# Optimization experiments

Hardware: AMD Instinct MI355X
Metric: run time of the kernel (lower is better)

Reference implementation:

```python
import math
import jax, jax.numpy as jnp
import numpy as np

H = 16  # head_count
D = 1024  # model_dim
DH = D // H  # dim_per_head = 64
PAD_IDX = 1


def setup_inputs() -> dict:
    key = jax.random.key(0)
    ks = jax.random.split(key, 16)
    B, L = 4, 512
    s = 0.02
    inp = {
        'key': jax.random.normal(ks[0], (B, L, D), jnp.float32),
        'value': jax.random.normal(ks[1], (B, L, D), jnp.float32),
        'query': jax.random.normal(ks[2], (B, L, D), jnp.float32),
        'ast_parents_matrix': jax.random.randint(ks[3], (B, L, L), 0, 200, jnp.int32),
        'mask': jnp.zeros((B, 1, L), jnp.bool_),
        'Wq': jax.random.normal(ks[4], (D, D), jnp.float32) * s,
        'bq': jnp.zeros((D,), jnp.float32),
        'Wk': jax.random.normal(ks[5], (D, D), jnp.float32) * s,
        'bk': jnp.zeros((D,), jnp.float32),
        'Wv': jax.random.normal(ks[6], (D, D), jnp.float32) * s,
        'bv': jnp.zeros((D,), jnp.float32),
        'Wo': jax.random.normal(ks[7], (D, D), jnp.float32) * s,
        'bo': jnp.zeros((D,), jnp.float32),
        'struct_emb': jax.random.normal(ks[8], (200, DH), jnp.float32).at[PAD_IDX].set(0.0),
        'value_emb': jax.random.normal(ks[9], (10000, DH), jnp.float32).at[PAD_IDX].set(0.0),
    }
    return inp


def _parent_embeddings(matrix, struct_emb, value_emb):
    # matrix: (B, Lq, K) int ids; even key positions use structure vocab, odd use value vocab
    B, Lq, K = matrix.shape
    s_ids = matrix[:, :, ::2]   # (B, Lq, ceil(K/2))
    v_ids = matrix[:, :, 1::2]  # (B, Lq, floor(K/2))
    emb_s = struct_emb[s_ids]   # (B, Lq, S, DH)
    emb_v = value_emb[v_ids]    # (B, Lq, V, DH)
    S = emb_s.shape[2]
    if emb_v.shape[2] != S:  # odd K: pad value stream by one zero slot, drop after interleave
        emb_v = jnp.concatenate([emb_v, jnp.zeros_like(emb_s[:, :, :1])], axis=2)
    pe = jnp.stack([emb_s, emb_v], axis=3).reshape(B, Lq, 2 * S, DH)
    return pe[:, :, :K, :]  # (B, Lq, K, DH)


def reference(key, value, query, ast_parents_matrix, mask,
              Wq, bq, Wk, bk, Wv, bv, Wo, bo, struct_emb, value_emb):
    B, L, _ = query.shape

    def shape(x):
        return x.reshape(B, -1, H, DH).transpose(0, 2, 1, 3)  # (B,H,L,DH)

    q = shape(query @ Wq + bq) / math.sqrt(DH)
    k = shape(key @ Wk + bk)
    v = shape(value @ Wv + bv)

    qk = jnp.einsum('bhid,bhjd->bhij', q, k)  # (B,H,L,L)

    pe = _parent_embeddings(ast_parents_matrix[:, :, :L], struct_emb, value_emb)
    score_ast = jnp.einsum('bhid,bijd->bhij', q, pe)

    scores = (qk + score_ast).astype(jnp.float32)
    scores = jnp.where(mask[:, None, :, :], -1e18, scores)  # mask: (B,1,L)->(B,1,1,L)
    attn = jax.nn.softmax(scores, axis=-1).astype(q.dtype)
    # dropout p=0.0 (eval) -> identity
    context = jnp.einsum('bhij,bhjd->bhid', attn, v)  # (B,H,L,DH)
    context = context.transpose(0, 2, 1, 3).reshape(B, L, D)
    output = context @ Wo + bo
    return output, attn
```

## Files before the change

### kernel.cpp

```cpp
#include <hip/hip_runtime.h>
#include <cstddef>

#define H 16
#define D 1024
#define DH 64
#define L 512

typedef __attribute__((ext_vector_type(8))) short bf16x8;
typedef __attribute__((ext_vector_type(4))) short bf16x4;
typedef __attribute__((ext_vector_type(4))) float f32x4;

__device__ inline short f2bf(float x) {
    union { float f; unsigned u; } c; c.f = x;
    unsigned r = (c.u + 0x7FFFu + ((c.u >> 16) & 1u)) >> 16;
    return (short)r;
}
__device__ inline float bf2f(short x) {
    union { float f; unsigned u; } c;
    c.u = ((unsigned)(unsigned short)x) << 16; return c.f;
}

__device__ inline void gload_lds16(const void* g, void* l) {
    __builtin_amdgcn_global_load_lds(
        (const __attribute__((address_space(1))) unsigned int*)g,
        (__attribute__((address_space(3))) unsigned int*)l,
        16, 0, 0);
}

struct CvtArgs { const float* src[5]; short* dst[5]; int n[5]; };

__global__ __launch_bounds__(256) void cvt_kernel(CvtArgs a) {
    int r = blockIdx.y;
    const float* s = a.src[r];
    short* d = a.dst[r];
    int n = a.n[r];
    int i = (blockIdx.x * 256 + threadIdx.x) * 8;
    if (i >= n) return;
    float4 x0 = *(const float4*)(s + i);
    float4 x1 = *(const float4*)(s + i + 4);
    bf16x8 o;
    o[0] = f2bf(x0.x); o[1] = f2bf(x0.y); o[2] = f2bf(x0.z); o[3] = f2bf(x0.w);
    o[4] = f2bf(x1.x); o[5] = f2bf(x1.y); o[6] = f2bf(x1.z); o[7] = f2bf(x1.w);
    *(bf16x8*)(d + i) = o;
}

struct WtArgs { const float* W[4]; short* T[4]; };

__global__ __launch_bounds__(256) void wtrans_kernel(WtArgs a) {
    const float* W = a.W[blockIdx.z];
    short* T = a.T[blockIdx.z];
    int idx = blockIdx.x * 256 + threadIdx.x;
    int n = idx & 1023;
    int k0 = (idx >> 10) << 3;
    bf16x8 o;
    #pragma unroll
    for (int kk = 0; kk < 8; ++kk)
        o[kk] = f2bf(W[(size_t)(k0 + kk) * 1024 + n]);
    *(bf16x8*)(T + (size_t)n * 1024 + k0) = o;
}

#define BM 128
#define BN 64
#define BKK 64

struct GemmBatch {
    const short* A[3]; const short* Bt[3]; const float* bias[3];
    void* out[3]; float scale[3]; int mode[3];
};

__global__ __launch_bounds__(256) void gemm_mfma_kernel(GemmBatch P, int M, int N, int K) {
    const int z = blockIdx.z;
    const short* __restrict__ A  = P.A[z];
    const short* __restrict__ Bt = P.Bt[z];
    const float* __restrict__ bias = P.bias[z];
    const float scale = P.scale[z];
    const int mode = P.mode[z];

    __shared__ short lds[(BM + BN) * BKK];
    short* As = lds;
    short* Bs = lds + BM * BKK;

    const int tid = threadIdx.x;
    const int wave = tid >> 6, lane = tid & 63;
    const int fm = lane & 15, quad = lane >> 4;
    const int m0 = blockIdx.y * BM, n0 = blockIdx.x * BN;

    int arow[4], acol[4];
    #pragma unroll
    for (int t = 0; t < 4; ++t) {
        int s = (wave * 4 + t) * 64 + lane;
        int row = s >> 3;
        int u = (s & 7) ^ (row & 7);
        arow[t] = row; acol[t] = u * 8;
    }
    int brow[2], bcol[2];
    #pragma unroll
    for (int t = 0; t < 2; ++t) {
        int s = (wave * 2 + t) * 64 + lane;
        int row = s >> 3;
        int u = (s & 7) ^ (row & 7);
        brow[t] = row; bcol[t] = u * 8;
    }

    int aoff[2][2], boff[4][2];
    #pragma unroll
    for (int mt = 0; mt < 2; ++mt)
        #pragma unroll
        for (int kst = 0; kst < 2; ++kst) {
            int row = wave * 32 + mt * 16 + fm;
            int u = quad + 4 * kst;
            aoff[mt][kst] = row * 64 + ((u ^ (row & 7)) * 8);
        }
    #pragma unroll
    for (int nt = 0; nt < 4; ++nt)
        #pragma unroll
        for (int kst = 0; kst < 2; ++kst) {
            int row = nt * 16 + fm;
            int u = quad + 4 * kst;
            boff[nt][kst] = row * 64 + ((u ^ (row & 7)) * 8);
        }

    f32x4 acc[2][4];
    #pragma unroll
    for (int mt = 0; mt < 2; ++mt)
        #pragma unroll
        for (int nt = 0; nt < 4; ++nt) acc[mt][nt] = (f32x4){0.f, 0.f, 0.f, 0.f};

    for (int k0 = 0; k0 < K; k0 += BKK) {
        __syncthreads();
        #pragma unroll
        for (int t = 0; t < 4; ++t)
            gload_lds16(A + (size_t)(m0 + arow[t]) * K + k0 + acol[t],
                        As + (wave * 4 + t) * 512);
        #pragma unroll
        for (int t = 0; t < 2; ++t)
            gload_lds16(Bt + (size_t)(n0 + brow[t]) * K + k0 + bcol[t],
                        Bs + (wave * 2 + t) * 512);
        __syncthreads();
        #pragma unroll
        for (int kst = 0; kst < 2; ++kst) {
            bf16x8 af[2], bfr[4];
            af[0] = *(const bf16x8*)(As + aoff[0][kst]);
            af[1] = *(const bf16x8*)(As + aoff[1][kst]);
            #pragma unroll
            for (int nt = 0; nt < 4; ++nt)
                bfr[nt] = *(const bf16x8*)(Bs + boff[nt][kst]);
            #pragma unroll
            for (int mt = 0; mt < 2; ++mt)
                #pragma unroll
                for (int nt = 0; nt < 4; ++nt)
                    acc[mt][nt] = __builtin_amdgcn_mfma_f32_16x16x32_bf16(
                        af[mt], bfr[nt], acc[mt][nt], 0, 0, 0);
        }
    }

    if (mode == 2) {
        __syncthreads();
        short (*T)[BM + 8] = (short(*)[BM + 8])&lds[0];
        #pragma unroll
        for (int mt = 0; mt < 2; ++mt)
            #pragma unroll
            for (int nt = 0; nt < 4; ++nt) {
                int nn = nt * 16 + fm;
                float bv = bias[n0 + nn];
                #pragma unroll
                for (int r = 0; r < 4; ++r) {
                    int mm = wave * 32 + mt * 16 + quad * 4 + r;
                    T[nn][mm] = f2bf((acc[mt][nt][r] + bv) * scale);
                }
            }
        __syncthreads();
        int b = m0 >> 9;
        int ibase = m0 & (L - 1);
        int hblk = n0 >> 6;
        int n = tid >> 2, seg = (tid & 3) * 32;
        short* dst = (short*)P.out[z] + (((size_t)(b * H + hblk) * DH + n) * L) + ibase + seg;
        #pragma unroll
        for (int c = 0; c < 4; ++c)
            *(bf16x8*)(dst + c * 8) = *(const bf16x8*)(&T[n][seg + c * 8]);
    } else {
        #pragma unroll
        for (int mt = 0; mt < 2; ++mt)
            #pragma unroll
            for (int nt = 0; nt < 4; ++nt) {
                int n = n0 + nt * 16 + fm;
                float bv = bias[n];
                #pragma unroll
                for (int r = 0; r < 4; ++r) {
                    int m = m0 + wave * 32 + mt * 16 + quad * 4 + r;
                    float val = (acc[mt][nt][r] + bv) * scale;
                    if (mode == 0) {
                        ((float*)P.out[z])[(size_t)m * N + n] = val;
                    } else {
                        int b = m >> 9, i = m & (L - 1);
                        int h = n >> 6, d = n & (DH - 1);
                        ((short*)P.out[z])[(((size_t)(b * H + h) * L + i) * DH) + d] = f2bf(val);
                    }
                }
            }
    }
}

__global__ __launch_bounds__(256) void ast_kernel(
    const short* __restrict__ Qb, const int* __restrict__ mat,
    const short* __restrict__ semb, const short* __restrict__ vemb,
    short* __restrict__ Sast)
{
    const int i = blockIdx.x, b = blockIdx.y;
    const int tid = threadIdx.x;
    const int wave = tid >> 6, lane = tid & 63;
    const int fm = lane & 15, quad = lane >> 4;
    __shared__ short Sl[H][L + 8];

    const short* qp = Qb + (((size_t)(b * H + fm) * L + i) * DH);
    bf16x8 a0 = *(const bf16x8*)(qp + quad * 8);
    bf16x8 a1 = *(const bf16x8*)(qp + 32 + quad * 8);

    const int* mrow = mat + ((size_t)b * L + i) * L;

    for (int jt = wave; jt < L / 16; jt += 4) {
        int j = jt * 16 + fm;
        int idx = mrow[j];
        const short* er = ((j & 1) ? vemb : semb) + (size_t)idx * DH;
        bf16x8 b0 = *(const bf16x8*)(er + quad * 8);
        bf16x8 b1 = *(const bf16x8*)(er + 32 + quad * 8);
        f32x4 c = {0.f, 0.f, 0.f, 0.f};
        c = __builtin_amdgcn_mfma_f32_16x16x32_bf16(a0, b0, c, 0, 0, 0);
        c = __builtin_amdgcn_mfma_f32_16x16x32_bf16(a1, b1, c, 0, 0, 0);
        #pragma unroll
        for (int r = 0; r < 4; ++r)
            Sl[quad * 4 + r][j] = f2bf(c[r]);
    }
    __syncthreads();
    int hh = tid >> 4, j0 = (tid & 15) * 32;
    short* dst = Sast + ((((size_t)b * L + i) * H + hh) * L) + j0;
    #pragma unroll
    for (int c = 0; c < 4; ++c)
        *(bf16x8*)(dst + c * 8) = *(const bf16x8*)(&Sl[hh][j0 + c * 8]);
}

__global__ __launch_bounds__(256) void attn_fused_kernel(
    const short* __restrict__ Qb, const short* __restrict__ Kb,
    const short* __restrict__ Vt, const short* __restrict__ Sast,
    const unsigned char* __restrict__ mask,
    float* __restrict__ attn, short* __restrict__ ctx)
{
    const int i0 = blockIdx.x * 16;
    const int h = blockIdx.y;
    const int b = blockIdx.z;
    const int tid = threadIdx.x;
    const int wave = tid >> 6, lane = tid & 63;
    const int fm = lane & 15, quad = lane >> 4;

    __shared__ short Pb[16][L + 8];
    __shared__ float red_m[4][16];
    __shared__ float red_l[4][16];

    const short* qp = Qb + (((size_t)(b * H + h) * L + i0 + fm) * DH);
    bf16x8 a0 = *(const bf16x8*)(qp + quad * 8);
    bf16x8 a1 = *(const bf16x8*)(qp + 32 + quad * 8);
    const short* Kbase = Kb + ((size_t)(b * H + h) * L) * DH;
    const short* Sb = Sast + (((size_t)b * L + i0) * H + h) * L;

    float s[8][4];
    float mx[4] = {-3.0e38f, -3.0e38f, -3.0e38f, -3.0e38f};

    #pragma unroll
    for (int t = 0; t < 8; ++t) {
        int jt = wave + t * 4;
        int j = jt * 16 + fm;
        const short* kr = Kbase + (size_t)j * DH;
        bf16x8 b0 = *(const bf16x8*)(kr + quad * 8);
        bf16x8 b1 = *(const bf16x8*)(kr + 32 + quad * 8);
        f32x4 c = {0.f, 0.f, 0.f, 0.f};
        c = __builtin_amdgcn_mfma_f32_16x16x32_bf16(a0, b0, c, 0, 0, 0);
        c = __builtin_amdgcn_mfma_f32_16x16x32_bf16(a1, b1, c, 0, 0, 0);
        bool mk = mask[(size_t)b * L + j] != 0;
        #pragma unroll
        for (int r = 0; r < 4; ++r) {
            int ir = quad * 4 + r;
            float sv = c[r] + bf2f(Sb[(size_t)ir * H * L + j]);
            sv = mk ? -1e18f : sv;
            s[t][r] = sv;
            mx[r] = fmaxf(mx[r], sv);
        }
    }

    #pragma unroll
    for (int off = 1; off <= 8; off <<= 1)
        #pragma unroll
        for (int r = 0; r < 4; ++r)
            mx[r] = fmaxf(mx[r], __shfl_xor(mx[r], off));
    if (fm == 0)
        #pragma unroll
        for (int r = 0; r < 4; ++r) red_m[wave][quad * 4 + r] = mx[r];
    __syncthreads();
    float M_[4];
    #pragma unroll
    for (int r = 0; r < 4; ++r) {
        int ir = quad * 4 + r;
        M_[r] = fmaxf(fmaxf(red_m[0][ir], red_m[1][ir]),
                      fmaxf(red_m[2][ir], red_m[3][ir]));
    }

    float sum[4] = {0.f, 0.f, 0.f, 0.f};
    #pragma unroll
    for (int t = 0; t < 8; ++t)
        #pragma unroll
        for (int r = 0; r < 4; ++r) {
            float e = __expf(s[t][r] - M_[r]);
            s[t][r] = e;
            sum[r] += e;
        }
    #pragma unroll
    for (int off = 1; off <= 8; off <<= 1)
        #pragma unroll
        for (int r = 0; r < 4; ++r)
            sum[r] += __shfl_xor(sum[r], off);
    if (fm == 0)
        #pragma unroll
        for (int r = 0; r < 4; ++r) red_l[wave][quad * 4 + r] = sum[r];
    __syncthreads();
    float inv[4];
    #pragma unroll
    for (int r = 0; r < 4; ++r) {
        int ir = quad * 4 + r;
        inv[r] = 1.f / (red_l[0][ir] + red_l[1][ir] + red_l[2][ir] + red_l[3][ir]);
    }

    #pragma unroll
    for (int t = 0; t < 8; ++t) {
        int j = (wave + t * 4) * 16 + fm;
        #pragma unroll
        for (int r = 0; r < 4; ++r) {
            int ir = quad * 4 + r;
            float p = s[t][r] * inv[r];
            attn[(((size_t)(b * H + h) * L + i0 + ir) * L) + j] = p;
            Pb[ir][j] = f2bf(p);
        }
    }
    __syncthreads();

    const short* Vb = Vt + (((size_t)(b * H + h) * DH + wave * 16 + fm) * L);
    f32x4 o = {0.f, 0.f, 0.f, 0.f};
    for (int ks = 0; ks < L; ks += 32) {
        bf16x8 pa = *(const bf16x8*)(&Pb[fm][ks + quad * 8]);
        bf16x8 vb = *(const bf16x8*)(Vb + ks + quad * 8);
        o = __builtin_amdgcn_mfma_f32_16x16x32_bf16(pa, vb, o, 0, 0, 0);
    }
    #pragma unroll
    for (int r = 0; r < 4; ++r)
        ctx[((size_t)b * L + i0 + quad * 4 + r) * D + h * DH + wave * 16 + fm] = f2bf(o[r]);
}

extern "C" void kernel_launch(void* const* d_in, const int* in_sizes, int n_in,
                              void* d_out, int out_size, void* d_ws, size_t ws_size,
                              hipStream_t stream) {
    const float* key_in   = (const float*)d_in[0];
    const float* value_in = (const float*)d_in[1];
    const float* query_in = (const float*)d_in[2];
    const int*   mat      = (const int*)d_in[3];
    const unsigned char* mask = (const unsigned char*)d_in[4];
    const float* Wq = (const float*)d_in[5];
    const float* bq = (const float*)d_in[6];
    const float* Wk = (const float*)d_in[7];
    const float* bk = (const float*)d_in[8];
    const float* Wv = (const float*)d_in[9];
    const float* bv = (const float*)d_in[10];
    const float* Wo = (const float*)d_in[11];
    const float* bo = (const float*)d_in[12];
    const float* struct_emb = (const float*)d_in[13];
    const float* value_emb  = (const float*)d_in[14];

    const int B = in_sizes[2] / (L * D);
    const int M = B * L;

    short* p = (short*)d_ws;
    short* xk  = p;  p += (size_t)M * D;
    short* xv  = p;  p += (size_t)M * D;
    short* xq  = p;  p += (size_t)M * D;
    short* WqT = p;  p += (size_t)D * D;
    short* WkT = p;  p += (size_t)D * D;
    short* WvT = p;  p += (size_t)D * D;
    short* WoT = p;  p += (size_t)D * D;
    short* semb = p; p += 16384;
    short* vemb = p; p += (size_t)in_sizes[14];
    short* Qb = p;   p += (size_t)M * D;
    short* Kb = p;   p += (size_t)M * D;
    short* Vt = p;   p += (size_t)M * D;
    short* Sast = p; p += (size_t)B * L * H * L;
    short* ctx = xk;

    float* out_p  = (float*)d_out;
    float* attn_p = out_p + (size_t)M * D;

    CvtArgs ca;
    ca.src[0] = key_in;     ca.dst[0] = xk;   ca.n[0] = M * D;
    ca.src[1] = value_in;   ca.dst[1] = xv;   ca.n[1] = M * D;
    ca.src[2] = query_in;   ca.dst[2] = xq;   ca.n[2] = M * D;
    ca.src[3] = struct_emb; ca.dst[3] = semb; ca.n[3] = in_sizes[13];
    ca.src[4] = value_emb;  ca.dst[4] = vemb; ca.n[4] = in_sizes[14];
    cvt_kernel<<<dim3((M * D) / 2048, 5), 256, 0, stream>>>(ca);

    WtArgs wa;
    wa.W[0] = Wq; wa.W[1] = Wk; wa.W[2] = Wv; wa.W[3] = Wo;
    wa.T[0] = WqT; wa.T[1] = WkT; wa.T[2] = WvT; wa.T[3] = WoT;
    wtrans_kernel<<<dim3(512, 1, 4), 256, 0, stream>>>(wa);

    GemmBatch qkv;
    qkv.A[0] = xq; qkv.Bt[0] = WqT; qkv.bias[0] = bq; qkv.out[0] = Qb; qkv.scale[0] = 0.125f; qkv.mode[0] = 1;
    qkv.A[1] = xk; qkv.Bt[1] = WkT; qkv.bias[1] = bk; qkv.out[1] = Kb; qkv.scale[1] = 1.0f;   qkv.mode[1] = 1;
    qkv.A[2] = xv; qkv.Bt[2] = WvT; qkv.bias[2] = bv; qkv.out[2] = Vt; qkv.scale[2] = 1.0f;   qkv.mode[2] = 2;
    gemm_mfma_kernel<<<dim3(D / BN, M / BM, 3), 256, 0, stream>>>(qkv, M, D, D);

    ast_kernel<<<dim3(L, B), 256, 0, stream>>>(Qb, mat, semb, vemb, Sast);

    attn_fused_kernel<<<dim3(L / 16, H, B), 256, 0, stream>>>(
        Qb, Kb, Vt, Sast, mask, attn_p, ctx);

    GemmBatch fin;
    fin.A[0] = ctx; fin.Bt[0] = WoT; fin.bias[0] = bo; fin.out[0] = out_p; fin.scale[0] = 1.0f; fin.mode[0] = 0;
    fin.A[1] = ctx; fin.Bt[1] = WoT; fin.bias[1] = bo; fin.out[1] = out_p; fin.scale[1] = 1.0f; fin.mode[1] = 0;
    fin.A[2] = ctx; fin.Bt[2] = WoT; fin.bias[2] = bo; fin.out[2] = out_p; fin.scale[2] = 1.0f; fin.mode[2] = 0;
    gemm_mfma_kernel<<<dim3(D / BN, M / BM, 1), 256, 0, stream>>>(fin, M, D, D);
}
```

Measured before the change: 242.0 us.

## Double attention row tile, stage AST scores in LDS, merge prep kernels, batch gathers

```diff
diff --git a/kernel.cpp b/kernel.cpp
--- a/kernel.cpp
+++ b/kernel.cpp
@@ -27,36 +27,38 @@
         16, 0, 0);
 }
 
-struct CvtArgs { const float* src[5]; short* dst[5]; int n[5]; };
-
-__global__ __launch_bounds__(256) void cvt_kernel(CvtArgs a) {
-    int r = blockIdx.y;
-    const float* s = a.src[r];
-    short* d = a.dst[r];
-    int n = a.n[r];
-    int i = (blockIdx.x * 256 + threadIdx.x) * 8;
-    if (i >= n) return;
-    float4 x0 = *(const float4*)(s + i);
-    float4 x1 = *(const float4*)(s + i + 4);
-    bf16x8 o;
-    o[0] = f2bf(x0.x); o[1] = f2bf(x0.y); o[2] = f2bf(x0.z); o[3] = f2bf(x0.w);
-    o[4] = f2bf(x1.x); o[5] = f2bf(x1.y); o[6] = f2bf(x1.z); o[7] = f2bf(x1.w);
-    *(bf16x8*)(d + i) = o;
-}
-
-struct WtArgs { const float* W[4]; short* T[4]; };
-
-__global__ __launch_bounds__(256) void wtrans_kernel(WtArgs a) {
-    const float* W = a.W[blockIdx.z];
-    short* T = a.T[blockIdx.z];
-    int idx = blockIdx.x * 256 + threadIdx.x;
-    int n = idx & 1023;
-    int k0 = (idx >> 10) << 3;
-    bf16x8 o;
-    #pragma unroll
-    for (int kk = 0; kk < 8; ++kk)
-        o[kk] = f2bf(W[(size_t)(k0 + kk) * 1024 + n]);
-    *(bf16x8*)(T + (size_t)n * 1024 + k0) = o;
+struct PrepArgs {
+    const float* csrc[5]; short* cdst[5]; int cn[5];
+    const float* W[4]; short* T[4];
+};
+
+__global__ __launch_bounds__(256) void prep_kernel(PrepArgs a) {
+    const int y = blockIdx.y;
+    if (y < 5) {
+        const float* s = a.csrc[y];
+        short* d = a.cdst[y];
+        int n = a.cn[y];
+        int i = (blockIdx.x * 256 + threadIdx.x) * 8;
+        if (i >= n) return;
+        float4 x0 = *(const float4*)(s + i);
+        float4 x1 = *(const float4*)(s + i + 4);
+        bf16x8 o;
+        o[0] = f2bf(x0.x); o[1] = f2bf(x0.y); o[2] = f2bf(x0.z); o[3] = f2bf(x0.w);
+        o[4] = f2bf(x1.x); o[5] = f2bf(x1.y); o[6] = f2bf(x1.z); o[7] = f2bf(x1.w);
+        *(bf16x8*)(d + i) = o;
+    } else {
+        const float* W = a.W[y - 5];
+        short* T = a.T[y - 5];
+        int idx = blockIdx.x * 256 + threadIdx.x;
+        if (idx >= 1024 * 128) return;
+        int n = idx & 1023;
+        int k0 = (idx >> 10) << 3;
+        bf16x8 o;
+        #pragma unroll
+        for (int kk = 0; kk < 8; ++kk)
+            o[kk] = f2bf(W[(size_t)(k0 + kk) * 1024 + n]);
+        *(bf16x8*)(T + (size_t)n * 1024 + k0) = o;
+    }
 }
 
 #define BM 128
@@ -218,12 +220,24 @@
 
     const int* mrow = mat + ((size_t)b * L + i) * L;
 
-    for (int jt = wave; jt < L / 16; jt += 4) {
-        int j = jt * 16 + fm;
-        int idx = mrow[j];
-        const short* er = ((j & 1) ? vemb : semb) + (size_t)idx * DH;
-        bf16x8 b0 = *(const bf16x8*)(er + quad * 8);
-        bf16x8 b1 = *(const bf16x8*)(er + 32 + quad * 8);
+    int idxs[8];
+    const short* ebase[8];
+    #pragma unroll
+    for (int t = 0; t < 8; ++t) {
+        int j = (wave + t * 4) * 16 + fm;
+        idxs[t] = mrow[j];
+    }
+    #pragma unroll
+    for (int t = 0; t < 8; ++t) {
+        int j = (wave + t * 4) * 16 + fm;
+        ebase[t] = ((j & 1) ? vemb : semb) + (size_t)idxs[t] * DH;
+    }
+
+    #pragma unroll
+    for (int t = 0; t < 8; ++t) {
+        int j = (wave + t * 4) * 16 + fm;
+        bf16x8 b0 = *(const bf16x8*)(ebase[t] + quad * 8);
+        bf16x8 b1 = *(const bf16x8*)(ebase[t] + 32 + quad * 8);
         f32x4 c = {0.f, 0.f, 0.f, 0.f};
         c = __builtin_amdgcn_mfma_f32_16x16x32_bf16(a0, b0, c, 0, 0, 0);
         c = __builtin_amdgcn_mfma_f32_16x16x32_bf16(a1, b1, c, 0, 0, 0);
@@ -245,112 +259,156 @@
     const unsigned char* __restrict__ mask,
     float* __restrict__ attn, short* __restrict__ ctx)
 {
-    const int i0 = blockIdx.x * 16;
+    const int i0 = blockIdx.x * 32;
     const int h = blockIdx.y;
     const int b = blockIdx.z;
     const int tid = threadIdx.x;
     const int wave = tid >> 6, lane = tid & 63;
     const int fm = lane & 15, quad = lane >> 4;
 
-    __shared__ short Pb[16][L + 8];
-    __shared__ float red_m[4][16];
-    __shared__ float red_l[4][16];
-
-    const short* qp = Qb + (((size_t)(b * H + h) * L + i0 + fm) * DH);
-    bf16x8 a0 = *(const bf16x8*)(qp + quad * 8);
-    bf16x8 a1 = *(const bf16x8*)(qp + 32 + quad * 8);
+    __shared__ short Pb[32][L + 8];
+    __shared__ float red_m[4][32];
+    __shared__ float red_l[4][32];
+
+    {
+        int r = tid >> 3, seg = (tid & 7) * 64;
+        const short* sp = Sast + ((((size_t)b * L + i0 + r) * H + h) * L) + seg;
+        #pragma unroll
+        for (int c = 0; c < 8; ++c)
+            *(bf16x8*)(&Pb[r][seg + c * 8]) = *(const bf16x8*)(sp + c * 8);
+    }
+
+    const short* qp0 = Qb + (((size_t)(b * H + h) * L + i0 + fm) * DH);
+    const short* qp1 = qp0 + 16 * DH;
+    bf16x8 a00 = *(const bf16x8*)(qp0 + quad * 8);
+    bf16x8 a01 = *(const bf16x8*)(qp0 + 32 + quad * 8);
+    bf16x8 a10 = *(const bf16x8*)(qp1 + quad * 8);
+    bf16x8 a11 = *(const bf16x8*)(qp1 + 32 + quad * 8);
     const short* Kbase = Kb + ((size_t)(b * H + h) * L) * DH;
-    const short* Sb = Sast + (((size_t)b * L + i0) * H + h) * L;
-
-    float s[8][4];
-    float mx[4] = {-3.0e38f, -3.0e38f, -3.0e38f, -3.0e38f};
+    __syncthreads();
+
+    float s[8][2][4];
+    float mx[2][4];
+    #pragma unroll
+    for (int rt = 0; rt < 2; ++rt)
+        #pragma unroll
+        for (int r = 0; r < 4; ++r) mx[rt][r] = -3.0e38f;
 
     #pragma unroll
     for (int t = 0; t < 8; ++t) {
-        int jt = wave + t * 4;
-        int j = jt * 16 + fm;
+        int j = (wave + t * 4) * 16 + fm;
         const short* kr = Kbase + (size_t)j * DH;
         bf16x8 b0 = *(const bf16x8*)(kr + quad * 8);
         bf16x8 b1 = *(const bf16x8*)(kr + 32 + quad * 8);
-        f32x4 c = {0.f, 0.f, 0.f, 0.f};
-        c = __builtin_amdgcn_mfma_f32_16x16x32_bf16(a0, b0, c, 0, 0, 0);
-        c = __builtin_amdgcn_mfma_f32_16x16x32_bf16(a1, b1, c, 0, 0, 0);
+        f32x4 c0 = {0.f, 0.f, 0.f, 0.f};
+        f32x4 c1 = {0.f, 0.f, 0.f, 0.f};
+        c0 = __builtin_amdgcn_mfma_f32_16x16x32_bf16(a00, b0, c0, 0, 0, 0);
+        c0 = __builtin_amdgcn_mfma_f32_16x16x32_bf16(a01, b1, c0, 0, 0, 0);
+        c1 = __builtin_amdgcn_mfma_f32_16x16x32_bf16(a10, b0, c1, 0, 0, 0);
+        c1 = __builtin_amdgcn_mfma_f32_16x16x32_bf16(a11, b1, c1, 0, 0, 0);
         bool mk = mask[(size_t)b * L + j] != 0;
         #pragma unroll
+        for (int rt = 0; rt < 2; ++rt) {
+            f32x4 c = rt ? c1 : c0;
+            #pragma unroll
+            for (int r = 0; r < 4; ++r) {
+                int ir = rt * 16 + quad * 4 + r;
+                float sv = c[r] + bf2f(Pb[ir][j]);
+                sv = mk ? -1e18f : sv;
+                s[t][rt][r] = sv;
+                mx[rt][r] = fmaxf(mx[rt][r], sv);
+            }
+        }
+    }
+
+    #pragma unroll
+    for (int off = 1; off <= 8; off <<= 1)
+        #pragma unroll
+        for (int rt = 0; rt < 2; ++rt)
+            #pragma unroll
+            for (int r = 0; r < 4; ++r)
+                mx[rt][r] = fmaxf(mx[rt][r], __shfl_xor(mx[rt][r], off));
+    if (fm == 0)
+        #pragma unroll
+        for (int rt = 0; rt < 2; ++rt)
+            #pragma unroll
+            for (int r = 0; r < 4; ++r)
+                red_m[wave][rt * 16 + quad * 4 + r] = mx[rt][r];
+    __syncthreads();
+    float M_[2][4];
+    #pragma unroll
+    for (int rt = 0; rt < 2; ++rt)
+        #pragma unroll
         for (int r = 0; r < 4; ++r) {
-            int ir = quad * 4 + r;
-            float sv = c[r] + bf2f(Sb[(size_t)ir * H * L + j]);
-            sv = mk ? -1e18f : sv;
-            s[t][r] = sv;
-            mx[r] = fmaxf(mx[r], sv);
-        }
-    }
-
+            int ir = rt * 16 + quad * 4 + r;
+            M_[rt][r] = fmaxf(fmaxf(red_m[0][ir], red_m[1][ir]),
+                              fmaxf(red_m[2][ir], red_m[3][ir]));
+        }
+
+    float sum[2][4] = {{0.f, 0.f, 0.f, 0.f}, {0.f, 0.f, 0.f, 0.f}};
+    #pragma unroll
+    for (int t = 0; t < 8; ++t)
+        #pragma unroll
+        for (int rt = 0; rt < 2; ++rt)
+            #pragma unroll
+            for (int r = 0; r < 4; ++r) {
+                float e = __expf(s[t][rt][r] - M_[rt][r]);
+                s[t][rt][r] = e;
+                sum[rt][r] += e;
+            }
     #pragma unroll
     for (int off = 1; off <= 8; off <<= 1)
         #pragma unroll
-        for (int r = 0; r < 4; ++r)
-            mx[r] = fmaxf(mx[r], __shfl_xor(mx[r], off));
+        for (int rt = 0; rt < 2; ++rt)
+            #pragma unroll
+            for (int r = 0; r < 4; ++r)
+                sum[rt][r] += __shfl_xor(sum[rt][r], off);
     if (fm == 0)
         #pragma unroll
-        for (int r = 0; r < 4; ++r) red_m[wave][quad * 4 + r] = mx[r];
+        for (int rt = 0; rt < 2; ++rt)
+            #pragma unroll
+            for (int r = 0; r < 4; ++r)
+                red_l[wave][rt * 16 + quad * 4 + r] = sum[rt][r];
     __syncthreads();
-    float M_[4];
-    #pragma unroll
-    for (int r = 0; r < 4; ++r) {
-        int ir = quad * 4 + r;
-        M_[r] = fmaxf(fmaxf(red_m[0][ir], red_m[1][ir]),
-                      fmaxf(red_m[2][ir], red_m[3][ir]));
-    }
-
-    float sum[4] = {0.f, 0.f, 0.f, 0.f};
-    #pragma unroll
-    for (int t = 0; t < 8; ++t)
+    float inv[2][4];
+    #pragma unroll
+    for (int rt = 0; rt < 2; ++rt)
         #pragma unroll
         for (int r = 0; r < 4; ++r) {
-            float e = __expf(s[t][r] - M_[r]);
-            s[t][r] = e;
-            sum[r] += e;
-        }
-    #pragma unroll
-    for (int off = 1; off <= 8; off <<= 1)
-        #pragma unroll
-        for (int r = 0; r < 4; ++r)
-            sum[r] += __shfl_xor(sum[r], off);
-    if (fm == 0)
-        #pragma unroll
-        for (int r = 0; r < 4; ++r) red_l[wave][quad * 4 + r] = sum[r];
-    __syncthreads();
-    float inv[4];
-    #pragma unroll
-    for (int r = 0; r < 4; ++r) {
-        int ir = quad * 4 + r;
-        inv[r] = 1.f / (red_l[0][ir] + red_l[1][ir] + red_l[2][ir] + red_l[3][ir]);
-    }
+            int ir = rt * 16 + quad * 4 + r;
+            inv[rt][r] = 1.f / (red_l[0][ir] + red_l[1][ir] + red_l[2][ir] + red_l[3][ir]);
+        }
 
     #pragma unroll
     for (int t = 0; t < 8; ++t) {
         int j = (wave + t * 4) * 16 + fm;
         #pragma unroll
-        for (int r = 0; r < 4; ++r) {
-            int ir = quad * 4 + r;
-            float p = s[t][r] * inv[r];
-            attn[(((size_t)(b * H + h) * L + i0 + ir) * L) + j] = p;
-            Pb[ir][j] = f2bf(p);
-        }
+        for (int rt = 0; rt < 2; ++rt)
+            #pragma unroll
+            for (int r = 0; r < 4; ++r) {
+                int ir = rt * 16 + quad * 4 + r;
+                float p = s[t][rt][r] * inv[rt][r];
+                attn[(((size_t)(b * H + h) * L + i0 + ir) * L) + j] = p;
+                Pb[ir][j] = f2bf(p);
+            }
     }
     __syncthreads();
 
     const short* Vb = Vt + (((size_t)(b * H + h) * DH + wave * 16 + fm) * L);
-    f32x4 o = {0.f, 0.f, 0.f, 0.f};
+    f32x4 o0 = {0.f, 0.f, 0.f, 0.f};
+    f32x4 o1 = {0.f, 0.f, 0.f, 0.f};
     for (int ks = 0; ks < L; ks += 32) {
-        bf16x8 pa = *(const bf16x8*)(&Pb[fm][ks + quad * 8]);
         bf16x8 vb = *(const bf16x8*)(Vb + ks + quad * 8);
-        o = __builtin_amdgcn_mfma_f32_16x16x32_bf16(pa, vb, o, 0, 0, 0);
-    }
-    #pragma unroll
-    for (int r = 0; r < 4; ++r)
-        ctx[((size_t)b * L + i0 + quad * 4 + r) * D + h * DH + wave * 16 + fm] = f2bf(o[r]);
+        bf16x8 p0 = *(const bf16x8*)(&Pb[fm][ks + quad * 8]);
+        bf16x8 p1 = *(const bf16x8*)(&Pb[16 + fm][ks + quad * 8]);
+        o0 = __builtin_amdgcn_mfma_f32_16x16x32_bf16(p0, vb, o0, 0, 0, 0);
+        o1 = __builtin_amdgcn_mfma_f32_16x16x32_bf16(p1, vb, o1, 0, 0, 0);
+    }
+    #pragma unroll
+    for (int r = 0; r < 4; ++r) {
+        ctx[((size_t)b * L + i0 + quad * 4 + r) * D + h * DH + wave * 16 + fm] = f2bf(o0[r]);
+        ctx[((size_t)b * L + i0 + 16 + quad * 4 + r) * D + h * DH + wave * 16 + fm] = f2bf(o1[r]);
+    }
 }
 
 extern "C" void kernel_launch(void* const* d_in, const int* in_sizes, int n_in,
@@ -394,18 +452,15 @@
     float* out_p  = (float*)d_out;
     float* attn_p = out_p + (size_t)M * D;
 
-    CvtArgs ca;
-    ca.src[0] = key_in;     ca.dst[0] = xk;   ca.n[0] = M * D;
-    ca.src[1] = value_in;   ca.dst[1] = xv;   ca.n[1] = M * D;
-    ca.src[2] = query_in;   ca.dst[2] = xq;   ca.n[2] = M * D;
-    ca.src[3] = struct_emb; ca.dst[3] = semb; ca.n[3] = in_sizes[13];
-    ca.src[4] = value_emb;  ca.dst[4] = vemb; ca.n[4] = in_sizes[14];
-    cvt_kernel<<<dim3((M * D) / 2048, 5), 256, 0, stream>>>(ca);
-
-    WtArgs wa;
-    wa.W[0] = Wq; wa.W[1] = Wk; wa.W[2] = Wv; wa.W[3] = Wo;
-    wa.T[0] = WqT; wa.T[1] = WkT; wa.T[2] = WvT; wa.T[3] = WoT;
-    wtrans_kernel<<<dim3(512, 1, 4), 256, 0, stream>>>(wa);
+    PrepArgs pa;
+    pa.csrc[0] = key_in;     pa.cdst[0] = xk;   pa.cn[0] = M * D;
+    pa.csrc[1] = value_in;   pa.cdst[1] = xv;   pa.cn[1] = M * D;
+    pa.csrc[2] = query_in;   pa.cdst[2] = xq;   pa.cn[2] = M * D;
+    pa.csrc[3] = struct_emb; pa.cdst[3] = semb; pa.cn[3] = in_sizes[13];
+    pa.csrc[4] = value_emb;  pa.cdst[4] = vemb; pa.cn[4] = in_sizes[14];
+    pa.W[0] = Wq; pa.W[1] = Wk; pa.W[2] = Wv; pa.W[3] = Wo;
+    pa.T[0] = WqT; pa.T[1] = WkT; pa.T[2] = WvT; pa.T[3] = WoT;
+    prep_kernel<<<dim3((M * D) / 2048, 9), 256, 0, stream>>>(pa);
 
     GemmBatch qkv;
     qkv.A[0] = xq; qkv.Bt[0] = WqT; qkv.bias[0] = bq; qkv.out[0] = Qb; qkv.scale[0] = 0.125f; qkv.mode[0] = 1;
@@ -415,7 +470,7 @@
 
     ast_kernel<<<dim3(L, B), 256, 0, stream>>>(Qb, mat, semb, vemb, Sast);
 
-    attn_fused_kernel<<<dim3(L / 16, H, B), 256, 0, stream>>>(
+    attn_fused_kernel<<<dim3(L / 32, H, B), 256, 0, stream>>>(
         Qb, Kb, Vt, Sast, mask, attn_p, ctx);
 
     GemmBatch fin;
```

New measurement: 246.1 us. About the same (+1.7%).
